# Performance work log

Hardware: AMD Instinct MI355X
Metric: run time of the kernel (lower is better)

Reference implementation:

```python
import jax, jax.numpy as jnp
import numpy as np

SIGMA = 2.0  # gaussian kernel std, matches init kwarg
N, H, W = 200, 448, 448
NUM_CLASSES = 80


def setup_inputs() -> dict:
    key = jax.random.key(0)
    k1, k2, k3 = jax.random.split(key, 3)
    seg_masks = (jax.random.uniform(k1, (N, H, W)) < 0.3).astype(jnp.float32)
    # scores in descending order (matrix_nms assumes sorted input)
    cate_scores = jnp.sort(jax.random.uniform(k2, (N,), dtype=jnp.float32))[::-1]
    cate_labels = jax.random.randint(k3, (N,), 0, NUM_CLASSES)
    return {"seg_masks": seg_masks, "cate_scores": cate_scores, "cate_labels": cate_labels}


def reference(seg_masks, cate_scores, cate_labels):
    n = seg_masks.shape[0]
    flat = seg_masks.reshape(n, -1).astype(jnp.float32)          # (n, HW)
    sum_masks = flat.sum(axis=1)                                  # (n,)
    inter = flat @ flat.T                                         # (n, n) mask intersection
    union = sum_masks[None, :] + sum_masks[:, None] - inter
    iou = jnp.triu(inter / union, k=1)                            # upper-tri IoU
    same_label = jnp.triu(
        (cate_labels[None, :] == cate_labels[:, None]).astype(jnp.float32), k=1
    )
    decay_iou = iou * same_label                                  # (n, n)
    # compensate IoU: per-candidate max overlap with a higher-scoring same-class mask
    compensate_iou = decay_iou.max(axis=0)                        # (n,)
    # gaussian decay: exp(-sigma*iou^2) / exp(-sigma*comp_i^2), min over rows
    decay_matrix = jnp.exp(SIGMA * (compensate_iou[:, None] ** 2 - decay_iou ** 2))
    decay_coefficient = decay_matrix.min(axis=0)                  # (n,)
    return cate_scores * decay_coefficient
```

## Files before the change

kernel.cpp:

```cpp
#include <hip/hip_runtime.h>
#include <cstdint>
#include <cstddef>

#define N_INST 200
#define HWPIX (448 * 448)
#define W64 3136
#define W16 12544
#define SIGMA 2.0f
#define NCHUNK 16
#define NTILE 325

#define P_SLAB  (N_INST * N_INST)
#define OFF_P   5017600
#define OFF_SP  (OFF_P + NCHUNK * P_SLAB * 4)
#define OFF_DT  (OFF_SP + NCHUNK * 256 * 4)
#define OFF_CMP (OFF_DT + N_INST * N_INST * 4)

__global__ void pack_kernel(const float* __restrict__ seg,
                            uint16_t* __restrict__ packed16) {
    const int mask = blockIdx.y;
    const int t    = threadIdx.x;
    const float4* s4 = (const float4*)(seg + (size_t)mask * HWPIX
                                           + (size_t)blockIdx.x * 4096);
    uint32_t m = 0;
#pragma unroll
    for (int s = 0; s < 4; ++s) {
        const float4 v = s4[s * 256 + t];
        uint32_t b = 0;
        b |= (v.x > 0.5f) ? 1u : 0u;
        b |= (v.y > 0.5f) ? 2u : 0u;
        b |= (v.z > 0.5f) ? 4u : 0u;
        b |= (v.w > 0.5f) ? 8u : 0u;
        m |= b << (4 * s);
    }
    packed16[(size_t)mask * W16 + blockIdx.x * 256 + t] = (uint16_t)m;
}

__global__ void pair_kernel(const uint64_t* __restrict__ packed,
                            int* __restrict__ P,
                            int* __restrict__ SP) {
    const int wt   = blockIdx.x * 4 + (threadIdx.x >> 6);
    const int lane = threadIdx.x & 63;
    const int t     = wt >> 4;
    const int chunk = wt & 15;

    int jt = (int)((sqrtf((float)(8 * t + 1)) - 1.0f) * 0.5f);
    while ((jt + 1) * (jt + 2) / 2 <= t) ++jt;
    while (jt * (jt + 1) / 2 > t) --jt;
    const int it = t - jt * (jt + 1) / 2;
    const int i0 = 8 * it, j0 = 8 * jt;

    const int ks = (chunk * 49) >> 4;
    const int ke = ((chunk + 1) * 49) >> 4;

    const uint64_t* A = packed + (size_t)i0 * W64;
    const uint64_t* B = packed + (size_t)j0 * W64;

    int c[64];
#pragma unroll
    for (int x = 0; x < 64; ++x) c[x] = 0;

    for (int kb = ks; kb < ke; ++kb) {
        const int k = kb * 64 + lane;
        uint64_t a[8], b[8];
#pragma unroll
        for (int r = 0; r < 8; ++r) { a[r] = A[k + r * W64]; b[r] = B[k + r * W64]; }
#pragma unroll
        for (int r = 0; r < 8; ++r)
#pragma unroll
            for (int cc = 0; cc < 8; ++cc)
                c[r * 8 + cc] += __popcll(a[r] & b[cc]);
    }

    int p[32];
#pragma unroll
    for (int m = 0; m < 32; ++m) p[m] = c[2 * m] + (c[2 * m + 1] << 16);
#pragma unroll
    for (int off = 1; off < 64; off <<= 1) {
#pragma unroll
        for (int m = 0; m < 32; ++m) p[m] += __shfl_xor(p[m], off, 64);
    }

    if (lane == 0) {
#pragma unroll
        for (int r = 0; r < 8; ++r) {
#pragma unroll
            for (int cc = 0; cc < 8; ++cc) {
                const int idx = r * 8 + cc;
                const int val = (idx & 1) ? (int)(((unsigned)p[idx >> 1]) >> 16)
                                          : (p[idx >> 1] & 0xFFFF);
                const int i = i0 + r, j = j0 + cc;
                if (i < j)       P[chunk * P_SLAB + j * N_INST + i] = val;
                else if (i == j) SP[chunk * 256 + i] = val;
            }
        }
    }
}

__global__ void iou_comp_kernel(const int* __restrict__ P,
                                const int* __restrict__ SP,
                                const int* __restrict__ labels,
                                float* __restrict__ DTf,
                                float* __restrict__ comp) {
    const int j = blockIdx.x;
    const int t = threadIdx.x;
    int sj = 0;
#pragma unroll
    for (int cch = 0; cch < NCHUNK; ++cch) sj += SP[cch * 256 + j];
    const int lj = labels[j];
    float m = 0.0f;
    for (int i = t; i < j; i += 64) {
        int inter = 0;
#pragma unroll
        for (int cch = 0; cch < NCHUNK; ++cch)
            inter += P[cch * P_SLAB + j * N_INST + i];
        int si = 0;
#pragma unroll
        for (int cch = 0; cch < NCHUNK; ++cch) si += SP[cch * 256 + i];
        const float iou = (float)inter / (float)(si + sj - inter);
        const float d = (labels[i] == lj) ? iou : 0.0f;
        DTf[j * N_INST + i] = d;
        m = fmaxf(m, d);
    }
#pragma unroll
    for (int off = 1; off < 64; off <<= 1) m = fmaxf(m, __shfl_xor(m, off, 64));
    if (t == 0) comp[j] = m;
}

__global__ void finalize_kernel(const float* __restrict__ DTf,
                                const float* __restrict__ comp,
                                const float* __restrict__ scores,
                                float* __restrict__ out) {
    const int j = blockIdx.x;
    const int t = threadIdx.x;
    const float* row = DTf + (size_t)j * N_INST;
    float mn = 3.4e38f;
    for (int i = t; i < N_INST; i += 64) {
        const float ci = comp[i];
        float v = ci * ci;
        if (i < j) { const float d = row[i]; v -= d * d; }
        mn = fminf(mn, v);
    }
#pragma unroll
    for (int off = 1; off < 64; off <<= 1) mn = fminf(mn, __shfl_xor(mn, off, 64));
    if (t == 0) out[j] = scores[j] * expf(SIGMA * mn);
}

extern "C" void kernel_launch(void* const* d_in, const int* in_sizes, int n_in,
                              void* d_out, int out_size, void* d_ws, size_t ws_size,
                              hipStream_t stream) {
    const float* seg    = (const float*)d_in[0];
    const float* scores = (const float*)d_in[1];
    const int*   labels = (const int*)d_in[2];
    float* out = (float*)d_out;

    uint64_t* packed   = (uint64_t*)d_ws;
    uint16_t* packed16 = (uint16_t*)d_ws;
    int*      P        = (int*)((char*)d_ws + OFF_P);
    int*      SP       = (int*)((char*)d_ws + OFF_SP);
    float*    DTf      = (float*)((char*)d_ws + OFF_DT);
    float*    comp     = (float*)((char*)d_ws + OFF_CMP);

    {
        dim3 grid(49, N_INST);
        pack_kernel<<<grid, 256, 0, stream>>>(seg, packed16);
    }
    pair_kernel<<<NTILE * NCHUNK / 4, 256, 0, stream>>>(packed, P, SP);
    iou_comp_kernel<<<N_INST, 64, 0, stream>>>(P, SP, labels, DTf, comp);
    finalize_kernel<<<N_INST, 64, 0, stream>>>(DTf, comp, scores, out);
}
```

Baseline: 253.7 us.

## Fuse all stages into one persistent kernel with grid barriers

Replaces the four kernel launches with a single persistent kernel of 512 blocks that uses a software grid barrier between the pack, pairwise-popcount, IoU/compensate and finalize phases. The K-split drops from 16 to 6 chunks, and the popcount loop uses 128-bit vector loads. The decay row is kept in registers rather than a DTf workspace round trip. This removes launch gaps and intermediate traffic, but relies on all 512 blocks being co-resident and adds barrier spin costs. The pack phase now runs on fewer threads with a grid-stride loop.

```diff
diff --git a/kernel.cpp b/kernel.cpp
--- a/kernel.cpp
+++ b/kernel.cpp
@@ -7,143 +7,198 @@
 #define W64 3136
 #define W16 12544
 #define SIGMA 2.0f
-#define NCHUNK 16
+#define NCHUNK 6
 #define NTILE 325
+#define NTASK (NTILE * NCHUNK)
+#define NBLK 512
+#define NTHREAD 256
 
 #define P_SLAB  (N_INST * N_INST)
 #define OFF_P   5017600
 #define OFF_SP  (OFF_P + NCHUNK * P_SLAB * 4)
-#define OFF_DT  (OFF_SP + NCHUNK * 256 * 4)
-#define OFF_CMP (OFF_DT + N_INST * N_INST * 4)
-
-__global__ void pack_kernel(const float* __restrict__ seg,
-                            uint16_t* __restrict__ packed16) {
-    const int mask = blockIdx.y;
-    const int t    = threadIdx.x;
-    const float4* s4 = (const float4*)(seg + (size_t)mask * HWPIX
-                                           + (size_t)blockIdx.x * 4096);
-    uint32_t m = 0;
-#pragma unroll
-    for (int s = 0; s < 4; ++s) {
-        const float4 v = s4[s * 256 + t];
-        uint32_t b = 0;
-        b |= (v.x > 0.5f) ? 1u : 0u;
-        b |= (v.y > 0.5f) ? 2u : 0u;
-        b |= (v.z > 0.5f) ? 4u : 0u;
-        b |= (v.w > 0.5f) ? 8u : 0u;
-        m |= b << (4 * s);
-    }
-    packed16[(size_t)mask * W16 + blockIdx.x * 256 + t] = (uint16_t)m;
-}
-
-__global__ void pair_kernel(const uint64_t* __restrict__ packed,
-                            int* __restrict__ P,
-                            int* __restrict__ SP) {
-    const int wt   = blockIdx.x * 4 + (threadIdx.x >> 6);
-    const int lane = threadIdx.x & 63;
-    const int t     = wt >> 4;
-    const int chunk = wt & 15;
-
-    int jt = (int)((sqrtf((float)(8 * t + 1)) - 1.0f) * 0.5f);
-    while ((jt + 1) * (jt + 2) / 2 <= t) ++jt;
-    while (jt * (jt + 1) / 2 > t) --jt;
-    const int it = t - jt * (jt + 1) / 2;
-    const int i0 = 8 * it, j0 = 8 * jt;
-
-    const int ks = (chunk * 49) >> 4;
-    const int ke = ((chunk + 1) * 49) >> 4;
-
-    const uint64_t* A = packed + (size_t)i0 * W64;
-    const uint64_t* B = packed + (size_t)j0 * W64;
-
-    int c[64];
-#pragma unroll
-    for (int x = 0; x < 64; ++x) c[x] = 0;
-
-    for (int kb = ks; kb < ke; ++kb) {
-        const int k = kb * 64 + lane;
-        uint64_t a[8], b[8];
-#pragma unroll
-        for (int r = 0; r < 8; ++r) { a[r] = A[k + r * W64]; b[r] = B[k + r * W64]; }
-#pragma unroll
-        for (int r = 0; r < 8; ++r)
-#pragma unroll
-            for (int cc = 0; cc < 8; ++cc)
-                c[r * 8 + cc] += __popcll(a[r] & b[cc]);
-    }
-
-    int p[32];
-#pragma unroll
-    for (int m = 0; m < 32; ++m) p[m] = c[2 * m] + (c[2 * m + 1] << 16);
-#pragma unroll
-    for (int off = 1; off < 64; off <<= 1) {
-#pragma unroll
-        for (int m = 0; m < 32; ++m) p[m] += __shfl_xor(p[m], off, 64);
-    }
-
-    if (lane == 0) {
-#pragma unroll
-        for (int r = 0; r < 8; ++r) {
-#pragma unroll
-            for (int cc = 0; cc < 8; ++cc) {
-                const int idx = r * 8 + cc;
-                const int val = (idx & 1) ? (int)(((unsigned)p[idx >> 1]) >> 16)
-                                          : (p[idx >> 1] & 0xFFFF);
-                const int i = i0 + r, j = j0 + cc;
-                if (i < j)       P[chunk * P_SLAB + j * N_INST + i] = val;
-                else if (i == j) SP[chunk * 256 + i] = val;
-            }
-        }
-    }
-}
-
-__global__ void iou_comp_kernel(const int* __restrict__ P,
-                                const int* __restrict__ SP,
-                                const int* __restrict__ labels,
-                                float* __restrict__ DTf,
-                                float* __restrict__ comp) {
-    const int j = blockIdx.x;
-    const int t = threadIdx.x;
-    int sj = 0;
-#pragma unroll
-    for (int cch = 0; cch < NCHUNK; ++cch) sj += SP[cch * 256 + j];
-    const int lj = labels[j];
-    float m = 0.0f;
-    for (int i = t; i < j; i += 64) {
-        int inter = 0;
-#pragma unroll
-        for (int cch = 0; cch < NCHUNK; ++cch)
-            inter += P[cch * P_SLAB + j * N_INST + i];
-        int si = 0;
-#pragma unroll
-        for (int cch = 0; cch < NCHUNK; ++cch) si += SP[cch * 256 + i];
-        const float iou = (float)inter / (float)(si + sj - inter);
-        const float d = (labels[i] == lj) ? iou : 0.0f;
-        DTf[j * N_INST + i] = d;
-        m = fmaxf(m, d);
-    }
-#pragma unroll
-    for (int off = 1; off < 64; off <<= 1) m = fmaxf(m, __shfl_xor(m, off, 64));
-    if (t == 0) comp[j] = m;
-}
-
-__global__ void finalize_kernel(const float* __restrict__ DTf,
-                                const float* __restrict__ comp,
-                                const float* __restrict__ scores,
-                                float* __restrict__ out) {
-    const int j = blockIdx.x;
-    const int t = threadIdx.x;
-    const float* row = DTf + (size_t)j * N_INST;
-    float mn = 3.4e38f;
-    for (int i = t; i < N_INST; i += 64) {
-        const float ci = comp[i];
-        float v = ci * ci;
-        if (i < j) { const float d = row[i]; v -= d * d; }
-        mn = fminf(mn, v);
-    }
-#pragma unroll
-    for (int off = 1; off < 64; off <<= 1) mn = fminf(mn, __shfl_xor(mn, off, 64));
-    if (t == 0) out[j] = scores[j] * expf(SIGMA * mn);
+#define OFF_CMP (OFF_SP + NCHUNK * 256 * 4)
+#define OFF_BAR (OFF_CMP + 1024)
+
+__device__ __forceinline__ void grid_barrier(int* bar) {
+    __syncthreads();
+    if (threadIdx.x == 0) {
+        __threadfence();
+        const int g = __hip_atomic_load(&bar[1], __ATOMIC_ACQUIRE,
+                                        __HIP_MEMORY_SCOPE_AGENT);
+        if (atomicAdd(&bar[0], 1) == NBLK - 1) {
+            atomicExch(&bar[0], 0);
+            __threadfence();
+            atomicAdd(&bar[1], 1);
+        } else {
+            while (__hip_atomic_load(&bar[1], __ATOMIC_ACQUIRE,
+                                     __HIP_MEMORY_SCOPE_AGENT) == g)
+                __builtin_amdgcn_s_sleep(1);
+        }
+        __threadfence();
+    }
+    __syncthreads();
+}
+
+__global__ void zero_bar_kernel(int* __restrict__ bar) {
+    bar[0] = 0; bar[1] = 0;
+}
+
+__global__ void __launch_bounds__(NTHREAD, 2)
+fused_kernel(const float* __restrict__ seg,
+             const float* __restrict__ scores,
+             const int* __restrict__ labels,
+             float* __restrict__ out,
+             uint64_t* __restrict__ packed,
+             int* __restrict__ P,
+             int* __restrict__ SP,
+             float* __restrict__ comp,
+             int* __restrict__ bar) {
+    const int tid  = blockIdx.x * NTHREAD + threadIdx.x;
+    const int wv   = tid >> 6;
+    const int lane = tid & 63;
+
+    {
+        uint16_t* packed16 = (uint16_t*)packed;
+        for (int w = tid; w < N_INST * W16; w += NBLK * NTHREAD) {
+            const int mask = w / W16;
+            const int widx = w - mask * W16;
+            const int bx = widx >> 8, t = widx & 255;
+            const float4* s4 = (const float4*)(seg + (size_t)mask * HWPIX
+                                                   + (size_t)bx * 4096);
+            uint32_t m = 0;
+#pragma unroll
+            for (int s = 0; s < 4; ++s) {
+                const float4 v = s4[s * 256 + t];
+                uint32_t b = 0;
+                b |= (v.x > 0.5f) ? 1u : 0u;
+                b |= (v.y > 0.5f) ? 2u : 0u;
+                b |= (v.z > 0.5f) ? 4u : 0u;
+                b |= (v.w > 0.5f) ? 8u : 0u;
+                m |= b << (4 * s);
+            }
+            packed16[w] = (uint16_t)m;
+        }
+    }
+    grid_barrier(bar);
+
+    if (wv < NTASK) {
+        const int t     = wv / NCHUNK;
+        const int chunk = wv - t * NCHUNK;
+        int jt = (int)((sqrtf((float)(8 * t + 1)) - 1.0f) * 0.5f);
+        while ((jt + 1) * (jt + 2) / 2 <= t) ++jt;
+        while (jt * (jt + 1) / 2 > t) --jt;
+        const int it = t - jt * (jt + 1) / 2;
+        const int i0 = 8 * it, j0 = 8 * jt;
+
+        const uint64_t* A = packed + (size_t)i0 * W64;
+        const uint64_t* B = packed + (size_t)j0 * W64;
+
+        int c[64];
+#pragma unroll
+        for (int x = 0; x < 64; ++x) c[x] = 0;
+
+        for (int pb = chunk * 4; pb < chunk * 4 + 4; ++pb) {
+            const int k2 = pb * 128 + lane * 2;
+            ulonglong2 a[8], b[8];
+#pragma unroll
+            for (int r = 0; r < 8; ++r) {
+                a[r] = *(const ulonglong2*)(A + (size_t)r * W64 + k2);
+                b[r] = *(const ulonglong2*)(B + (size_t)r * W64 + k2);
+            }
+#pragma unroll
+            for (int r = 0; r < 8; ++r)
+#pragma unroll
+                for (int cc = 0; cc < 8; ++cc)
+                    c[r * 8 + cc] += __popcll(a[r].x & b[cc].x)
+                                   + __popcll(a[r].y & b[cc].y);
+        }
+        if (chunk == 5) {
+            const int k = 3072 + lane;
+            uint64_t a[8], b[8];
+#pragma unroll
+            for (int r = 0; r < 8; ++r) {
+                a[r] = A[(size_t)r * W64 + k];
+                b[r] = B[(size_t)r * W64 + k];
+            }
+#pragma unroll
+            for (int r = 0; r < 8; ++r)
+#pragma unroll
+                for (int cc = 0; cc < 8; ++cc)
+                    c[r * 8 + cc] += __popcll(a[r] & b[cc]);
+        }
+
+        int p[32];
+#pragma unroll
+        for (int m = 0; m < 32; ++m) p[m] = c[2 * m] + (c[2 * m + 1] << 16);
+#pragma unroll
+        for (int off = 1; off < 64; off <<= 1) {
+#pragma unroll
+            for (int m = 0; m < 32; ++m) p[m] += __shfl_xor(p[m], off, 64);
+        }
+
+        if (lane == 0) {
+#pragma unroll
+            for (int r = 0; r < 8; ++r) {
+#pragma unroll
+                for (int cc = 0; cc < 8; ++cc) {
+                    const int idx = r * 8 + cc;
+                    const int val = (idx & 1) ? (int)(((unsigned)p[idx >> 1]) >> 16)
+                                              : (p[idx >> 1] & 0xFFFF);
+                    const int i = i0 + r, j = j0 + cc;
+                    if (i < j)       P[chunk * P_SLAB + j * N_INST + i] = val;
+                    else if (i == j) SP[chunk * 256 + i] = val;
+                }
+            }
+        }
+    }
+    grid_barrier(bar);
+
+    float d[4] = {0.0f, 0.0f, 0.0f, 0.0f};
+    const int j = wv;
+    if (j < N_INST) {
+        int sj = 0;
+#pragma unroll
+        for (int cch = 0; cch < NCHUNK; ++cch) sj += SP[cch * 256 + j];
+        const int lj = labels[j];
+        float m = 0.0f;
+#pragma unroll
+        for (int q = 0; q < 4; ++q) {
+            const int i = lane + 64 * q;
+            if (i < j) {
+                int inter = 0;
+#pragma unroll
+                for (int cch = 0; cch < NCHUNK; ++cch)
+                    inter += P[cch * P_SLAB + j * N_INST + i];
+                int si = 0;
+#pragma unroll
+                for (int cch = 0; cch < NCHUNK; ++cch) si += SP[cch * 256 + i];
+                const float iou = (float)inter / (float)(si + sj - inter);
+                d[q] = (labels[i] == lj) ? iou : 0.0f;
+                m = fmaxf(m, d[q]);
+            }
+        }
+#pragma unroll
+        for (int off = 1; off < 64; off <<= 1)
+            m = fmaxf(m, __shfl_xor(m, off, 64));
+        if (lane == 0) comp[j] = m;
+    }
+    grid_barrier(bar);
+
+    if (j < N_INST) {
+        float mn = 3.4e38f;
+#pragma unroll
+        for (int q = 0; q < 4; ++q) {
+            const int i = lane + 64 * q;
+            if (i < N_INST) {
+                const float ci = comp[i];
+                mn = fminf(mn, ci * ci - d[q] * d[q]);
+            }
+        }
+#pragma unroll
+        for (int off = 1; off < 64; off <<= 1)
+            mn = fminf(mn, __shfl_xor(mn, off, 64));
+        if (lane == 0) out[j] = scores[j] * expf(SIGMA * mn);
+    }
 }
 
 extern "C" void kernel_launch(void* const* d_in, const int* in_sizes, int n_in,
@@ -154,18 +209,13 @@
     const int*   labels = (const int*)d_in[2];
     float* out = (float*)d_out;
 
-    uint64_t* packed   = (uint64_t*)d_ws;
-    uint16_t* packed16 = (uint16_t*)d_ws;
-    int*      P        = (int*)((char*)d_ws + OFF_P);
-    int*      SP       = (int*)((char*)d_ws + OFF_SP);
-    float*    DTf      = (float*)((char*)d_ws + OFF_DT);
-    float*    comp     = (float*)((char*)d_ws + OFF_CMP);
-
-    {
-        dim3 grid(49, N_INST);
-        pack_kernel<<<grid, 256, 0, stream>>>(seg, packed16);
-    }
-    pair_kernel<<<NTILE * NCHUNK / 4, 256, 0, stream>>>(packed, P, SP);
-    iou_comp_kernel<<<N_INST, 64, 0, stream>>>(P, SP, labels, DTf, comp);
-    finalize_kernel<<<N_INST, 64, 0, stream>>>(DTf, comp, scores, out);
-}
+    uint64_t* packed = (uint64_t*)d_ws;
+    int*      P      = (int*)((char*)d_ws + OFF_P);
+    int*      SP     = (int*)((char*)d_ws + OFF_SP);
+    float*    comp   = (float*)((char*)d_ws + OFF_CMP);
+    int*      bar    = (int*)((char*)d_ws + OFF_BAR);
+
+    zero_bar_kernel<<<1, 1, 0, stream>>>(bar);
+    fused_kernel<<<NBLK, NTHREAD, 0, stream>>>(seg, scores, labels, out,
+                                               packed, P, SP, comp, bar);
+}
```

Measured after the change: 474.6 us. 87.1% more time.
